# Optimization experiments

Hardware: AMD Instinct MI355X
Metric: run time of the kernel (lower is better)

## Reference

```python
import jax, jax.numpy as jnp
from jax import lax
import numpy as np

P = 128      # stored adversarial patch resolution
WIN = 256    # max pasted-patch extent (>= max patch_size = sqrt(300*300*0.4) ~ 190)
MINH = 60.0  # min_patch_height
H, W, B, N = 896, 896, 8, 24


def _bilinear(img, ys, xs):
    """Bilinearly sample img [h,w,c] on the grid ys x xs -> [len(ys), len(xs), c]."""
    h, w = img.shape[0], img.shape[1]
    ys = jnp.clip(ys, 0.0, h - 1.0)
    xs = jnp.clip(xs, 0.0, w - 1.0)
    y0 = jnp.floor(ys); x0 = jnp.floor(xs)
    y0i = y0.astype(jnp.int32); x0i = x0.astype(jnp.int32)
    y1i = jnp.minimum(y0i + 1, h - 1); x1i = jnp.minimum(x0i + 1, w - 1)
    wy = (ys - y0)[:, None, None]; wx = (xs - x0)[None, :, None]
    v00 = img[y0i][:, x0i]; v01 = img[y0i][:, x1i]
    v10 = img[y1i][:, x0i]; v11 = img[y1i][:, x1i]
    return (1 - wy) * ((1 - wx) * v00 + wx * v01) + wy * ((1 - wx) * v10 + wx * v11)


def setup_inputs() -> dict:
    key = jax.random.key(0)
    ks = jax.random.split(key, 8)
    ymin = jax.random.uniform(ks[0], (B, N), minval=0.0, maxval=H - 320.0)
    bh = jax.random.uniform(ks[1], (B, N), minval=80.0, maxval=300.0)
    xmin = jax.random.uniform(ks[2], (B, N), minval=0.0, maxval=W - 320.0)
    bw = jax.random.uniform(ks[3], (B, N), minval=80.0, maxval=300.0)
    boxes = jnp.stack([ymin, xmin, ymin + bh, xmin + bw], axis=-1)
    images = jax.random.uniform(ks[4], (B, H, W, 3))
    patch = jax.random.uniform(ks[5], (P, P, 3))
    Ws = jax.random.normal(ks[6], (2, 1)) * 0.5
    bs = jnp.zeros((1,), jnp.float32)
    Wg = jax.random.normal(ks[7], (2, P * P)) * 0.5
    bg = jnp.zeros((P * P,), jnp.float32)
    return {"boxes": boxes, "images": images, "patch": patch,
            "Ws": Ws, "bs": bs, "Wg": Wg, "bg": bg}


def reference(boxes, images, patch, Ws, bs, Wg, bg):
    Bx, Hx, Wx, C = images.shape
    Hf, Wf = float(Hx), float(Wx)
    mu_p = patch.mean((0, 1)); sd_p = patch.std((0, 1)) + 1e-6

    def per_image(image, bxs):
        bh = (bxs[:, 2] - bxs[:, 0]) / Hf
        bw = (bxs[:, 3] - bxs[:, 1]) / Wf
        feats = jnp.stack([bh, bw], axis=-1)                      # [N,2]
        scales = jax.nn.sigmoid(feats @ Ws + bs)[:, 0] * 0.4
        # Patcher.create (vectorized over boxes)
        h = bxs[:, 2] - bxs[:, 0]; w = bxs[:, 3] - bxs[:, 1]
        ps = jnp.floor(jnp.sqrt(h * w * scales))                  # square patch side
        oy = bxs[:, 0] + h / 2.0; ox = bxs[:, 1] + w / 2.0
        ymp = jnp.maximum(oy - ps / 2.0, 0.0)
        xmp = jnp.maximum(ox - ps / 2.0, 0.0)
        ymp = jnp.where(ymp + ps > Hf, Hf - ps, ymp)
        xmp = jnp.where(xmp + ps > Wf, Wf - ps, xmp)
        pboxes = jnp.stack([ymp, xmp, ps, ps], axis=-1)           # [N,4]
        valid = ps > MINH                                          # filter-by-mask
        masks = jax.nn.sigmoid(feats @ Wg + bg).reshape(-1, P, P, 1)  # gen masks
        img_p = jnp.pad(image, ((0, WIN), (0, WIN), (0, 0)))

        def body(carry, inp):
            imgc, bgl = carry
            pbox, mask, vld = inp
            yi = pbox[0].astype(jnp.int32); xi = pbox[1].astype(jnp.int32)
            ph = pbox[2].astype(jnp.int32); pw = pbox[3].astype(jnp.int32)
            phf = jnp.maximum(ph, 1).astype(jnp.float32)
            pwf = jnp.maximum(pw, 1).astype(jnp.float32)
            # crop background region -> fixed PxP
            ys = yi.astype(jnp.float32) + (jnp.arange(P, dtype=jnp.float32) + 0.5) * phf / P - 0.5
            xs = xi.astype(jnp.float32) + (jnp.arange(P, dtype=jnp.float32) + 0.5) * pwf / P - 0.5
            patch_bg = _bilinear(imgc, ys, xs)                    # [P,P,C]
            # histogram (moment) matching of patch to local background
            mu_b = patch_bg.mean((0, 1)); sd_b = patch_bg.std((0, 1)) + 1e-6
            matched = (patch - mu_p) / sd_p * sd_b + mu_b
            blended = jnp.where(mask > 0.5, matched, patch_bg)
            r = jnp.arange(WIN, dtype=jnp.float32)
            sy = (r + 0.5) * P / phf - 0.5
            sx = (r + 0.5) * P / pwf - 0.5
            im_win = _bilinear(blended, sy, sx)
            win = lax.dynamic_slice(imgc, (yi, xi, 0), (WIN, WIN, imgc.shape[-1]))
            inside = (jnp.arange(WIN)[:, None] < ph) & (jnp.arange(WIN)[None, :] < pw) & vld
            upd = jnp.where(inside[..., None], im_win, win)
            imgc = lax.dynamic_update_slice(imgc, upd, (yi, xi, 0))
            bgl = bgl + jnp.where(vld, mask.mean(), 0.0)          # generator.bg_loss
            return (imgc, bgl), None

        (img_p, bgl), _ = lax.scan(body, (img_p, jnp.zeros((), jnp.float32)),
                                   (pboxes, masks, valid))
        # scale loss over valid boxes: mean + 0.5*variance
        vf = valid.astype(jnp.float32)
        n = jnp.maximum(vf.sum(), 1.0)
        m = (scales * vf).sum() / n
        var = (vf * (scales - m) ** 2).sum() / n
        return img_p[:Hx, :Wx], bgl + m + 0.5 * var

    out, losses = jax.vmap(per_image)(images, boxes)
    return out, losses.sum()
```

## Files before the change

### kernel.cpp

```cpp
#include <hip/hip_runtime.h>

#define PPX  128
#define PP2  16384
#define IMH  896
#define IMW  896
#define NB   24
#define NI   8
#define HP   1152
#define WP   1152
#define MAXG 6
#define NMB  (NI*NB*8)
#define NCPY 2048
#define M1   12

#define WS_BOX  8
#define WS_MASK 2048
#define WS_SCH  100352
#define WS_LIST 100608
#define WS_MSUM 101760
#define WS_PART 103424
#define WS_PBG  140288

__device__ __forceinline__ void box_geom(const float* __restrict__ bx,
    const float* __restrict__ Wsc, const float* __restrict__ bsc,
    float& scale, float& ps, int& yi, int& xi, int& ph, int& vld)
{
  float ya=bx[0], xa=bx[1], yb=bx[2], xb=bx[3];
  float bh=(yb-ya)/(float)IMH, bw=(xb-xa)/(float)IMW;
  float z = bh*Wsc[0]+bw*Wsc[1]+bsc[0];
  float sig = 1.f/(1.f+expf(-z));
  scale = sig*0.4f;
  float h=yb-ya, w=xb-xa;
  ps = floorf(sqrtf((h*w)*scale));
  float oy=ya+h*0.5f, ox=xa+w*0.5f;
  float ymp=fmaxf(oy-ps*0.5f,0.f), xmp=fmaxf(ox-ps*0.5f,0.f);
  if (ymp+ps>(float)IMH) ymp=(float)IMH-ps;
  if (xmp+ps>(float)IMW) xmp=(float)IMW-ps;
  yi=(int)ymp; xi=(int)xmp; ph=(int)ps;
  vld = (ps>60.f) ? 1 : 0;
}

__device__ __forceinline__ void analytic3(int rr, int cc, float phf,
    const float* __restrict__ pbg1, const float* __restrict__ patch,
    const unsigned* msk, const float* ab, float v[3])
{
  float sy = ((rr + 0.5f)*128.0f)/phf - 0.5f;
  float sx = ((cc + 0.5f)*128.0f)/phf - 0.5f;
  sy = fminf(fmaxf(sy, 0.f), 127.f);
  sx = fminf(fmaxf(sx, 0.f), 127.f);
  float fy0 = floorf(sy), fx0 = floorf(sx);
  int py0 = (int)fy0, px0 = (int)fx0;
  int py1 = py0 + 1 < 127 ? py0 + 1 : 127;
  int px1 = px0 + 1 < 127 ? px0 + 1 : 127;
  float wy = sy - fy0, wx = sx - fx0;
  int i00 = (py0<<7)+px0, i01 = (py0<<7)+px1, i10 = (py1<<7)+px0, i11 = (py1<<7)+px1;
  bool m00 = (msk[i00>>5] >> (i00&31)) & 1u;
  bool m01 = (msk[i01>>5] >> (i01&31)) & 1u;
  bool m10 = (msk[i10>>5] >> (i10&31)) & 1u;
  bool m11 = (msk[i11>>5] >> (i11&31)) & 1u;
  #pragma unroll
  for (int ch = 0; ch < 3; ++ch) {
    float a = ab[ch], be = ab[3+ch];
    float t00 = m00 ? patch[i00*3+ch]*a + be : pbg1[i00*3+ch];
    float t01 = m01 ? patch[i01*3+ch]*a + be : pbg1[i01*3+ch];
    float t10 = m10 ? patch[i10*3+ch]*a + be : pbg1[i10*3+ch];
    float t11 = m11 ? patch[i11*3+ch]*a + be : pbg1[i11*3+ch];
    v[ch] = (1.f-wy)*((1.f-wx)*t00 + wx*t01) + wy*((1.f-wx)*t10 + wx*t11);
  }
}

__device__ __forceinline__ void crop_plain(
    const float* __restrict__ src, float* __restrict__ ws, int b, int n, int blk,
    float (*s_red)[6])
{
  const int tid = threadIdx.x;
  const int* bi = (const int*)(ws + WS_BOX + (b*NB + n)*8);
  const int yi = bi[2], xi = bi[3], ph = bi[4];
  const float phf = (float)(ph > 1 ? ph : 1);
  float* __restrict__ pbg = ws + WS_PBG + (size_t)(b*NB + n)*PP2*3;
  float sm[3] = {0,0,0}, sq[3] = {0,0,0};
  #pragma unroll
  for (int k = 0; k < 2; ++k) {
    int idx = blk*512 + k*256 + tid;
    int py = idx >> 7, px = idx & 127;
    float ys = ((float)yi + (py + 0.5f)*phf*(1.0f/PPX)) - 0.5f;
    float xs = ((float)xi + (px + 0.5f)*phf*(1.0f/PPX)) - 0.5f;
    ys = fminf(fmaxf(ys, 0.f), (float)(HP-1));
    xs = fminf(fmaxf(xs, 0.f), (float)(WP-1));
    float fy0 = floorf(ys), fx0 = floorf(xs);
    int y0 = (int)fy0, x0 = (int)fx0;
    int y1 = y0 + 1 < HP-1 ? y0 + 1 : HP-1;
    int x1 = x0 + 1 < WP-1 ? x0 + 1 : WP-1;
    float wy = ys - fy0, wx = xs - fx0;
    bool y0i = y0 < IMH, y1i = y1 < IMH, x0i = x0 < IMW, x1i = x1 < IMW;
    const float* r0 = src + (size_t)y0*IMW*3;
    const float* r1 = src + (size_t)y1*IMW*3;
    #pragma unroll
    for (int c = 0; c < 3; ++c) {
      float v00 = (y0i && x0i) ? r0[x0*3+c] : 0.f;
      float v01 = (y0i && x1i) ? r0[x1*3+c] : 0.f;
      float v10 = (y1i && x0i) ? r1[x0*3+c] : 0.f;
      float v11 = (y1i && x1i) ? r1[x1*3+c] : 0.f;
      float v = (1.f-wy)*((1.f-wx)*v00 + wx*v01) + wy*((1.f-wx)*v10 + wx*v11);
      pbg[idx*3+c] = v;
      sm[c] += v; sq[c] += v*v;
    }
  }
  float vals[6] = {sm[0],sm[1],sm[2],sq[0],sq[1],sq[2]};
  #pragma unroll
  for (int off = 32; off; off >>= 1)
    #pragma unroll
    for (int k = 0; k < 6; ++k) vals[k] += __shfl_down(vals[k], off);
  int wid = tid >> 6;
  __syncthreads();
  if ((tid & 63) == 0)
    for (int k = 0; k < 6; ++k) s_red[wid][k] = vals[k];
  __syncthreads();
  if (tid == 0) {
    float* part = ws + WS_PART + (size_t)((b*NB + n)*32 + blk)*6;
    for (int k = 0; k < 6; ++k)
      part[k] = s_red[0][k] + s_red[1][k] + s_red[2][k] + s_red[3][k];
  }
}

__global__ __launch_bounds__(256) void sched_k(
    const float* __restrict__ boxes,
    const float* __restrict__ Wsc, const float* __restrict__ bsc,
    const float* __restrict__ patch, float* __restrict__ ws)
{
  const int tid = threadIdx.x;
  if (blockIdx.x == 1) {
    __shared__ float s_red6[256][6];
    float s0=0,s1=0,s2=0,q0=0,q1=0,q2=0;
    for (int i = tid; i < PP2; i += 256) {
      float a = patch[i*3+0], b = patch[i*3+1], c = patch[i*3+2];
      s0+=a; s1+=b; s2+=c; q0+=a*a; q1+=b*b; q2+=c*c;
    }
    s_red6[tid][0]=s0; s_red6[tid][1]=s1; s_red6[tid][2]=s2;
    s_red6[tid][3]=q0; s_red6[tid][4]=q1; s_red6[tid][5]=q2;
    __syncthreads();
    for (int s = 128; s > 0; s >>= 1) {
      if (tid < s)
        for (int k=0;k<6;++k) s_red6[tid][k] += s_red6[tid+s][k];
      __syncthreads();
    }
    if (tid == 0) {
      for (int c=0;c<3;++c) {
        float mu  = s_red6[0][c]   * (1.0f/PP2);
        float var = s_red6[0][3+c] * (1.0f/PP2) - mu*mu;
        float sd  = sqrtf(fmaxf(var, 0.f)) + 1e-6f;
        ws[c] = mu; ws[3+c] = sd;
      }
    }
    return;
  }
  __shared__ int g_yi[NI*NB], g_xi[NI*NB], g_ph[NI*NB], g_vl[NI*NB];
  if (tid < NI*NB) {
    float scale, ps; int yi, xi, ph, vld;
    box_geom(boxes + tid*4, Wsc, bsc, scale, ps, yi, xi, ph, vld);
    g_yi[tid]=yi; g_xi[tid]=xi; g_ph[tid]=ph; g_vl[tid]=vld;
    float* bst = ws + WS_BOX + tid*8;
    bst[0] = scale;
    bst[1] = ps;
    ((int*)bst)[2] = yi;
    ((int*)bst)[3] = xi;
    ((int*)bst)[4] = ph;
    bst[5] = vld ? 1.f : 0.f;
  }
  __syncthreads();
  if (tid < NI) {
    unsigned* sch = ((unsigned*)ws) + WS_SCH + tid*32;
    unsigned* lst = ((unsigned*)ws) + WS_LIST + tid*(MAXG*NB);
    int lv[NB];
    int cnt[MAXG];
    for (int L = 0; L < MAXG; ++L) cnt[L] = 0;
    for (int n = 0; n < NB; ++n) {
      int idx = tid*NB + n;
      if (!g_vl[idx]) { lv[n] = -1; sch[n] = 255u; continue; }
      int y0 = g_yi[idx]-2, y1 = g_yi[idx]+g_ph[idx]+3;
      int x0 = g_xi[idx]-2, x1 = g_xi[idx]+g_ph[idx]+3;
      int L = 0;
      for (int m = 0; m < n; ++m) {
        if (lv[m] < 0) continue;
        int mi = tid*NB + m;
        int my0 = g_yi[mi]-2, my1 = g_yi[mi]+g_ph[mi]+3;
        int mx0 = g_xi[mi]-2, mx1 = g_xi[mi]+g_ph[mi]+3;
        if (y0 < my1 && my0 < y1 && x0 < mx1 && mx0 < x1)
          L = max(L, lv[m] + 1);
      }
      lv[n] = L;
      sch[n] = (unsigned)L;
      if (L < MAXG) lst[L*NB + cnt[L]++] = (unsigned)n;
    }
    for (int L = 0; L < MAXG; ++L) sch[24 + L] = (unsigned)cnt[L];
  }
}

__global__ __launch_bounds__(256) void first_k(
    float* __restrict__ out, const float* __restrict__ images,
    const float* __restrict__ boxes,
    const float* __restrict__ Wg, const float* __restrict__ bgv,
    float* __restrict__ ws)
{
  const int bid = blockIdx.x, tid = threadIdx.x;
  if (bid < NCPY) {
    const float4* src4 = (const float4*)images;
    float4* dst4 = (float4*)out;
    const int n4 = NI*IMH*IMW*3/4;
    for (int i = bid*256 + tid; i < n4; i += NCPY*256) dst4[i] = src4[i];
    return;
  }
  if (bid < NCPY + NMB) {
    const int w = bid - NCPY;
    const int bn = w >> 3, q = w & 7;
    float bh = (boxes[bn*4+2]-boxes[bn*4+0])/(float)IMH;
    float bw = (boxes[bn*4+3]-boxes[bn*4+1])/(float)IMW;
    unsigned* mwords = ((unsigned*)ws) + WS_MASK + bn*512;
    float lsum = 0.f;
    const int lane = tid & 63;
    #pragma unroll
    for (int i = 0; i < 8; ++i) {
      int p = q*2048 + i*256 + tid;
      float zz = bh*Wg[p] + bw*Wg[PP2 + p] + bgv[p];
      lsum += 1.0f / (1.0f + expf(-zz));
      unsigned long long m = __ballot(zz > 0.0f);
      if (lane == 0) {
        int base = p >> 5;
        mwords[base]   = (unsigned)(m & 0xffffffffULL);
        mwords[base+1] = (unsigned)(m >> 32);
      }
    }
    #pragma unroll
    for (int off = 32; off; off >>= 1) lsum += __shfl_down(lsum, off);
    __shared__ float s_r[4];
    if ((tid & 63) == 0) s_r[tid >> 6] = lsum;
    __syncthreads();
    if (tid == 0) ws[WS_MSUM + bn*8 + q] = s_r[0] + s_r[1] + s_r[2] + s_r[3];
    return;
  }
  const int w = bid - NCPY - NMB;
  const int b = w / (M1*32);
  const int rem = w - b*(M1*32);
  const int j = rem >> 5, blk = rem & 31;
  __shared__ float s_red[4][6];
  __shared__ int s_cn[NB];
  __shared__ int s_cc;
  const unsigned* sch = ((const unsigned*)ws) + WS_SCH + b*32;
  if (tid == 0) s_cc = (int)sch[24 + 0];
  __syncthreads();
  const int cc = s_cc;
  if (j >= cc) return;
  if (tid < cc) s_cn[tid] = (int)(((const unsigned*)ws) + WS_LIST + b*(MAXG*NB))[tid];
  __syncthreads();
  const float* src = images + (size_t)b*IMH*IMW*3;
  for (int jj = j; jj < cc; jj += M1)
    crop_plain(src, ws, b, s_cn[jj], blk, s_red);
}

__global__ __launch_bounds__(256) void crop_k(
    float* __restrict__ out, float* __restrict__ ws, int L, int M)
{
  const int bid = blockIdx.x, tid = threadIdx.x;
  const int b = bid / (M*32);
  const int rem = bid - b*(M*32);
  const int j = rem >> 5, blk = rem & 31;
  __shared__ float s_red[4][6];
  __shared__ int s_cn[NB];
  __shared__ int s_cc;
  const unsigned* sch = ((const unsigned*)ws) + WS_SCH + b*32;
  if (tid == 0) s_cc = (int)sch[24 + L];
  __syncthreads();
  const int cc = s_cc;
  if (j >= cc) return;
  if (tid < cc) s_cn[tid] = (int)(((const unsigned*)ws) + WS_LIST + b*(MAXG*NB))[L*NB + tid];
  __syncthreads();
  const float* src = out + (size_t)b*IMH*IMW*3;
  for (int jj = j; jj < cc; jj += M)
    crop_plain(src, ws, b, s_cn[jj], blk, s_red);
}

__global__ __launch_bounds__(256) void paste_k(
    float* __restrict__ out, const float* __restrict__ patch,
    float* __restrict__ ws, int L, int M)
{
  const int bid = blockIdx.x, tid = threadIdx.x;
  if (bid >= NI*M*32) {
    if (tid == 0) {
      float total = 0.f;
      for (int b = 0; b < NI; ++b) {
        float sum_s = 0.f, cnt = 0.f, bgl = 0.f;
        for (int n = 0; n < NB; ++n) {
          const float* bst = ws + WS_BOX + (b*NB + n)*8;
          float v = bst[5];
          float msum = 0.f;
          for (int q = 0; q < 8; ++q) msum += ws[WS_MSUM + (b*NB + n)*8 + q];
          sum_s += bst[0]*v; cnt += v; bgl += (msum*(1.0f/PP2))*v;
        }
        float nn = fmaxf(cnt, 1.0f);
        float m = sum_s / nn;
        float var = 0.f;
        for (int n = 0; n < NB; ++n) {
          const float* bst = ws + WS_BOX + (b*NB + n)*8;
          float d = bst[0] - m;
          var += bst[5]*d*d;
        }
        var /= nn;
        total += bgl + m + 0.5f*var;
      }
      out[(size_t)NI*IMH*IMW*3] = total;
    }
    return;
  }
  const int b = bid / (M*32);
  const int rem = bid - b*(M*32);
  const int j = rem >> 5, r = rem & 31;
  __shared__ int s_cp;
  __shared__ int s_pn[NB];
  __shared__ float s_ab[6];
  __shared__ unsigned s_mask[512];
  const unsigned* sch = ((const unsigned*)ws) + WS_SCH + b*32;
  if (tid == 0) s_cp = (int)sch[24 + L];
  __syncthreads();
  const int cp = s_cp;
  if (j >= cp) return;
  if (tid < cp) s_pn[tid] = (int)(((const unsigned*)ws) + WS_LIST + b*(MAXG*NB))[L*NB + tid];
  __syncthreads();
  float* __restrict__ img = out + (size_t)b*IMH*IMW*3;

  for (int jj = j; jj < cp; jj += M) {
    const int n = s_pn[jj];
    if (tid < 32) {
      const float* part = ws + WS_PART + (size_t)((b*NB + n)*32 + tid)*6;
      float v[6];
      #pragma unroll
      for (int k = 0; k < 6; ++k) v[k] = part[k];
      #pragma unroll
      for (int off = 16; off; off >>= 1)
        #pragma unroll
        for (int k = 0; k < 6; ++k) v[k] += __shfl_down(v[k], off, 32);
      if (tid == 0) {
        #pragma unroll
        for (int c = 0; c < 3; ++c) {
          float mu  = v[c]   * (1.0f/PP2);
          float var = v[3+c] * (1.0f/PP2) - mu*mu;
          float sd  = sqrtf(fmaxf(var, 0.f)) + 1e-6f;
          float alpha = sd / ws[3+c];
          s_ab[c]   = alpha;
          s_ab[3+c] = mu - ws[c]*alpha;
        }
      }
    }
    {
      const unsigned* mwords = ((const unsigned*)ws) + WS_MASK + (b*NB + n)*512;
      s_mask[tid]       = mwords[tid];
      s_mask[tid + 256] = mwords[tid + 256];
    }
    __syncthreads();
    const int* bi = (const int*)(ws + WS_BOX + (b*NB + n)*8);
    const int yi = bi[2], xi = bi[3], ph = bi[4];
    const float phf = (float)(ph > 1 ? ph : 1);
    const float* pbgp = ws + WS_PBG + (size_t)(b*NB + n)*PP2*3;
    const int tot = ph*ph;
    const int chunk = (tot + 31) / 32;
    const int i0 = r*chunk;
    const int i1 = min(tot, i0 + chunk);
    for (int idx = i0 + tid; idx < i1; idx += 256) {
      int rr = (int)((unsigned)idx / (unsigned)ph);
      int cx = idx - rr*ph;
      float v[3];
      analytic3(rr, cx, phf, pbgp, patch, s_mask, s_ab, v);
      float* dst = img + ((size_t)(yi + rr)*IMW + (xi + cx))*3;
      dst[0] = v[0]; dst[1] = v[1]; dst[2] = v[2];
    }
    __syncthreads();
  }
}

__global__ __launch_bounds__(256) void fallback_k(
    float* __restrict__ out, const float* __restrict__ patch, float* __restrict__ ws)
{
  const int b = blockIdx.x, tid = threadIdx.x;
  const unsigned* sch = ((const unsigned*)ws) + WS_SCH + b*32;
  float* __restrict__ img = out + (size_t)b*IMH*IMW*3;
  float* __restrict__ pbg = ws + WS_PBG + (size_t)(b*NB + 0)*PP2*3;
  __shared__ float s_red6[256][6];
  __shared__ float s_ab[6];
  __shared__ unsigned s_mask[512];

  for (int n = 0; n < NB; ++n) {
    unsigned g = sch[n];
    if (g < (unsigned)MAXG || g == 255u) continue;
    const float* bst = ws + WS_BOX + (b*NB + n)*8;
    const int yi = ((const int*)bst)[2];
    const int xi = ((const int*)bst)[3];
    const int ph = ((const int*)bst)[4];
    const float phf = (float)(ph > 1 ? ph : 1);

    float sm[3]={0,0,0}, sq[3]={0,0,0};
    for (int k = 0; k < PP2/256; ++k) {
      int idx = k*256 + tid;
      int py = idx >> 7, px = idx & 127;
      float ys = ((float)yi + (py + 0.5f)*phf*(1.0f/PPX)) - 0.5f;
      float xs = ((float)xi + (px + 0.5f)*phf*(1.0f/PPX)) - 0.5f;
      ys = fminf(fmaxf(ys, 0.f), (float)(HP-1));
      xs = fminf(fmaxf(xs, 0.f), (float)(WP-1));
      float fy0 = floorf(ys), fx0 = floorf(xs);
      int y0 = (int)fy0, x0 = (int)fx0;
      int y1 = y0 + 1 < HP-1 ? y0 + 1 : HP-1;
      int x1 = x0 + 1 < WP-1 ? x0 + 1 : WP-1;
      float wy = ys - fy0, wx = xs - fx0;
      bool y0i = y0 < IMH, y1i = y1 < IMH, x0i = x0 < IMW, x1i = x1 < IMW;
      const float* r0 = img + (size_t)y0*IMW*3;
      const float* r1 = img + (size_t)y1*IMW*3;
      #pragma unroll
      for (int c = 0; c < 3; ++c) {
        float v00 = (y0i && x0i) ? r0[x0*3+c] : 0.f;
        float v01 = (y0i && x1i) ? r0[x1*3+c] : 0.f;
        float v10 = (y1i && x0i) ? r1[x0*3+c] : 0.f;
        float v11 = (y1i && x1i) ? r1[x1*3+c] : 0.f;
        float v = (1.f-wy)*((1.f-wx)*v00 + wx*v01) + wy*((1.f-wx)*v10 + wx*v11);
        pbg[idx*3+c] = v;
        sm[c] += v; sq[c] += v*v;
      }
    }
    s_red6[tid][0]=sm[0]; s_red6[tid][1]=sm[1]; s_red6[tid][2]=sm[2];
    s_red6[tid][3]=sq[0]; s_red6[tid][4]=sq[1]; s_red6[tid][5]=sq[2];
    __syncthreads();
    for (int s2 = 128; s2 > 0; s2 >>= 1) {
      if (tid < s2)
        for (int k=0;k<6;++k) s_red6[tid][k] += s_red6[tid+s2][k];
      __syncthreads();
    }
    if (tid == 0) {
      for (int c=0;c<3;++c) {
        float mu  = s_red6[0][c]   * (1.0f/PP2);
        float var = s_red6[0][3+c] * (1.0f/PP2) - mu*mu;
        float sd  = sqrtf(fmaxf(var, 0.f)) + 1e-6f;
        float alpha = sd / ws[3+c];
        s_ab[c]   = alpha;
        s_ab[3+c] = mu - ws[c]*alpha;
      }
    }
    {
      const unsigned* mwords = ((const unsigned*)ws) + WS_MASK + (b*NB + n)*512;
      s_mask[tid]       = mwords[tid];
      s_mask[tid + 256] = mwords[tid + 256];
    }
    __syncthreads();
    const int tot = ph*ph;
    for (int idx = tid; idx < tot; idx += 256) {
      int rr = (int)((unsigned)idx / (unsigned)ph);
      int cc = idx - rr*ph;
      float v[3];
      analytic3(rr, cc, phf, pbg, patch, s_mask, s_ab, v);
      float* dst = img + ((size_t)(yi + rr)*IMW + (xi + cc))*3;
      dst[0] = v[0]; dst[1] = v[1]; dst[2] = v[2];
    }
    __syncthreads();
  }
}

extern "C" void kernel_launch(void* const* d_in, const int* in_sizes, int n_in,
                              void* d_out, int out_size, void* d_ws, size_t ws_size,
                              hipStream_t stream) {
  const float* boxes  = (const float*)d_in[0];
  const float* images = (const float*)d_in[1];
  const float* patch  = (const float*)d_in[2];
  const float* Wsc    = (const float*)d_in[3];
  const float* bsc    = (const float*)d_in[4];
  const float* Wg     = (const float*)d_in[5];
  const float* bgv    = (const float*)d_in[6];
  float* out = (float*)d_out;
  float* ws  = (float*)d_ws;

  sched_k<<<2, 256, 0, stream>>>(boxes, Wsc, bsc, patch, ws);
  first_k<<<NCPY + NMB + NI*M1*32, 256, 0, stream>>>(out, images, boxes, Wg, bgv, ws);
  paste_k<<<NI*M1*32 + 1, 256, 0, stream>>>(out, patch, ws, 0, M1);
  crop_k <<<NI*8*32, 256, 0, stream>>>(out, ws, 1, 8);
  paste_k<<<NI*8*32, 256, 0, stream>>>(out, patch, ws, 1, 8);
  crop_k <<<NI*4*32, 256, 0, stream>>>(out, ws, 2, 4);
  paste_k<<<NI*4*32, 256, 0, stream>>>(out, patch, ws, 2, 4);
  crop_k <<<NI*2*32, 256, 0, stream>>>(out, ws, 3, 2);
  paste_k<<<NI*2*32, 256, 0, stream>>>(out, patch, ws, 3, 2);
  crop_k <<<NI*2*32, 256, 0, stream>>>(out, ws, 4, 2);
  paste_k<<<NI*2*32, 256, 0, stream>>>(out, patch, ws, 4, 2);
  crop_k <<<NI*2*32, 256, 0, stream>>>(out, ws, 5, 2);
  paste_k<<<NI*2*32, 256, 0, stream>>>(out, patch, ws, 5, 2);
  fallback_k<<<NI, 256, 0, stream>>>(out, patch, ws);
}
```

Measured before the change: 200.8 us.

## Fuse crop and paste per level into single 1024-thread step kernel

Merges the scheduling kernel into the copy/mask kernel, and fuses each level's crop (background resample plus statistics) and paste into one step kernel. That kernel uses one 1024-thread block per box instead of 32 crop blocks and 32 paste blocks. This removes the partial-sum workspace round trip and cuts the launch count roughly in half. In exchange, each box now gets a single block, so far fewer blocks are in flight per level, and the per-level block counts were also retuned.

```diff
diff --git a/kernel.cpp b/kernel.cpp
--- a/kernel.cpp
+++ b/kernel.cpp
@@ -9,17 +9,15 @@
 #define HP   1152
 #define WP   1152
 #define MAXG 6
-#define NMB  (NI*NB*8)
+#define NMB  (NI*NB)
 #define NCPY 2048
-#define M1   12
 
 #define WS_BOX  8
 #define WS_MASK 2048
 #define WS_SCH  100352
 #define WS_LIST 100608
 #define WS_MSUM 101760
-#define WS_PART 103424
-#define WS_PBG  140288
+#define WS_PBG  103424
 
 __device__ __forceinline__ void box_geom(const float* __restrict__ bx,
     const float* __restrict__ Wsc, const float* __restrict__ bsc,
@@ -69,67 +67,15 @@
   }
 }
 
-__device__ __forceinline__ void crop_plain(
-    const float* __restrict__ src, float* __restrict__ ws, int b, int n, int blk,
-    float (*s_red)[6])
-{
-  const int tid = threadIdx.x;
-  const int* bi = (const int*)(ws + WS_BOX + (b*NB + n)*8);
-  const int yi = bi[2], xi = bi[3], ph = bi[4];
-  const float phf = (float)(ph > 1 ? ph : 1);
-  float* __restrict__ pbg = ws + WS_PBG + (size_t)(b*NB + n)*PP2*3;
-  float sm[3] = {0,0,0}, sq[3] = {0,0,0};
-  #pragma unroll
-  for (int k = 0; k < 2; ++k) {
-    int idx = blk*512 + k*256 + tid;
-    int py = idx >> 7, px = idx & 127;
-    float ys = ((float)yi + (py + 0.5f)*phf*(1.0f/PPX)) - 0.5f;
-    float xs = ((float)xi + (px + 0.5f)*phf*(1.0f/PPX)) - 0.5f;
-    ys = fminf(fmaxf(ys, 0.f), (float)(HP-1));
-    xs = fminf(fmaxf(xs, 0.f), (float)(WP-1));
-    float fy0 = floorf(ys), fx0 = floorf(xs);
-    int y0 = (int)fy0, x0 = (int)fx0;
-    int y1 = y0 + 1 < HP-1 ? y0 + 1 : HP-1;
-    int x1 = x0 + 1 < WP-1 ? x0 + 1 : WP-1;
-    float wy = ys - fy0, wx = xs - fx0;
-    bool y0i = y0 < IMH, y1i = y1 < IMH, x0i = x0 < IMW, x1i = x1 < IMW;
-    const float* r0 = src + (size_t)y0*IMW*3;
-    const float* r1 = src + (size_t)y1*IMW*3;
-    #pragma unroll
-    for (int c = 0; c < 3; ++c) {
-      float v00 = (y0i && x0i) ? r0[x0*3+c] : 0.f;
-      float v01 = (y0i && x1i) ? r0[x1*3+c] : 0.f;
-      float v10 = (y1i && x0i) ? r1[x0*3+c] : 0.f;
-      float v11 = (y1i && x1i) ? r1[x1*3+c] : 0.f;
-      float v = (1.f-wy)*((1.f-wx)*v00 + wx*v01) + wy*((1.f-wx)*v10 + wx*v11);
-      pbg[idx*3+c] = v;
-      sm[c] += v; sq[c] += v*v;
-    }
-  }
-  float vals[6] = {sm[0],sm[1],sm[2],sq[0],sq[1],sq[2]};
-  #pragma unroll
-  for (int off = 32; off; off >>= 1)
-    #pragma unroll
-    for (int k = 0; k < 6; ++k) vals[k] += __shfl_down(vals[k], off);
-  int wid = tid >> 6;
-  __syncthreads();
-  if ((tid & 63) == 0)
-    for (int k = 0; k < 6; ++k) s_red[wid][k] = vals[k];
-  __syncthreads();
-  if (tid == 0) {
-    float* part = ws + WS_PART + (size_t)((b*NB + n)*32 + blk)*6;
-    for (int k = 0; k < 6; ++k)
-      part[k] = s_red[0][k] + s_red[1][k] + s_red[2][k] + s_red[3][k];
-  }
-}
-
-__global__ __launch_bounds__(256) void sched_k(
+__global__ __launch_bounds__(256) void first_k(
+    float* __restrict__ out, const float* __restrict__ images,
     const float* __restrict__ boxes,
     const float* __restrict__ Wsc, const float* __restrict__ bsc,
+    const float* __restrict__ Wg, const float* __restrict__ bgv,
     const float* __restrict__ patch, float* __restrict__ ws)
 {
-  const int tid = threadIdx.x;
-  if (blockIdx.x == 1) {
+  const int bid = blockIdx.x, tid = threadIdx.x;
+  if (bid == NCPY) {
     __shared__ float s_red6[256][6];
     float s0=0,s1=0,s2=0,q0=0,q1=0,q2=0;
     for (int i = tid; i < PP2; i += 256) {
@@ -154,65 +100,52 @@
     }
     return;
   }
-  __shared__ int g_yi[NI*NB], g_xi[NI*NB], g_ph[NI*NB], g_vl[NI*NB];
-  if (tid < NI*NB) {
-    float scale, ps; int yi, xi, ph, vld;
-    box_geom(boxes + tid*4, Wsc, bsc, scale, ps, yi, xi, ph, vld);
-    g_yi[tid]=yi; g_xi[tid]=xi; g_ph[tid]=ph; g_vl[tid]=vld;
-    float* bst = ws + WS_BOX + tid*8;
-    bst[0] = scale;
-    bst[1] = ps;
-    ((int*)bst)[2] = yi;
-    ((int*)bst)[3] = xi;
-    ((int*)bst)[4] = ph;
-    bst[5] = vld ? 1.f : 0.f;
-  }
-  __syncthreads();
-  if (tid < NI) {
-    unsigned* sch = ((unsigned*)ws) + WS_SCH + tid*32;
-    unsigned* lst = ((unsigned*)ws) + WS_LIST + tid*(MAXG*NB);
-    int lv[NB];
-    int cnt[MAXG];
-    for (int L = 0; L < MAXG; ++L) cnt[L] = 0;
-    for (int n = 0; n < NB; ++n) {
-      int idx = tid*NB + n;
-      if (!g_vl[idx]) { lv[n] = -1; sch[n] = 255u; continue; }
-      int y0 = g_yi[idx]-2, y1 = g_yi[idx]+g_ph[idx]+3;
-      int x0 = g_xi[idx]-2, x1 = g_xi[idx]+g_ph[idx]+3;
-      int L = 0;
-      for (int m = 0; m < n; ++m) {
-        if (lv[m] < 0) continue;
-        int mi = tid*NB + m;
-        int my0 = g_yi[mi]-2, my1 = g_yi[mi]+g_ph[mi]+3;
-        int mx0 = g_xi[mi]-2, mx1 = g_xi[mi]+g_ph[mi]+3;
-        if (y0 < my1 && my0 < y1 && x0 < mx1 && mx0 < x1)
-          L = max(L, lv[m] + 1);
-      }
-      lv[n] = L;
-      sch[n] = (unsigned)L;
-      if (L < MAXG) lst[L*NB + cnt[L]++] = (unsigned)n;
-    }
-    for (int L = 0; L < MAXG; ++L) sch[24 + L] = (unsigned)cnt[L];
-  }
-}
-
-__global__ __launch_bounds__(256) void first_k(
-    float* __restrict__ out, const float* __restrict__ images,
-    const float* __restrict__ boxes,
-    const float* __restrict__ Wg, const float* __restrict__ bgv,
-    float* __restrict__ ws)
-{
-  const int bid = blockIdx.x, tid = threadIdx.x;
-  if (bid < NCPY) {
-    const float4* src4 = (const float4*)images;
-    float4* dst4 = (float4*)out;
-    const int n4 = NI*IMH*IMW*3/4;
-    for (int i = bid*256 + tid; i < n4; i += NCPY*256) dst4[i] = src4[i];
+  if (bid == NCPY + 1) {
+    __shared__ int g_yi[NI*NB], g_xi[NI*NB], g_ph[NI*NB], g_vl[NI*NB];
+    if (tid < NI*NB) {
+      float scale, ps; int yi, xi, ph, vld;
+      box_geom(boxes + tid*4, Wsc, bsc, scale, ps, yi, xi, ph, vld);
+      g_yi[tid]=yi; g_xi[tid]=xi; g_ph[tid]=ph; g_vl[tid]=vld;
+      float* bst = ws + WS_BOX + tid*8;
+      bst[0] = scale;
+      bst[1] = ps;
+      ((int*)bst)[2] = yi;
+      ((int*)bst)[3] = xi;
+      ((int*)bst)[4] = ph;
+      bst[5] = vld ? 1.f : 0.f;
+    }
+    __syncthreads();
+    if (tid < NI) {
+      unsigned* sch = ((unsigned*)ws) + WS_SCH + tid*32;
+      unsigned* lst = ((unsigned*)ws) + WS_LIST + tid*(MAXG*NB);
+      int lv[NB];
+      int cnt[MAXG];
+      for (int L = 0; L < MAXG; ++L) cnt[L] = 0;
+      for (int n = 0; n < NB; ++n) {
+        int idx = tid*NB + n;
+        if (!g_vl[idx]) { lv[n] = -1; sch[n] = 255u; continue; }
+        int y0 = g_yi[idx]-2, y1 = g_yi[idx]+g_ph[idx]+3;
+        int x0 = g_xi[idx]-2, x1 = g_xi[idx]+g_ph[idx]+3;
+        int L = 0;
+        for (int m = 0; m < n; ++m) {
+          if (lv[m] < 0) continue;
+          int mi = tid*NB + m;
+          int my0 = g_yi[mi]-2, my1 = g_yi[mi]+g_ph[mi]+3;
+          int mx0 = g_xi[mi]-2, mx1 = g_xi[mi]+g_ph[mi]+3;
+          if (y0 < my1 && my0 < y1 && x0 < mx1 && mx0 < x1)
+            L = max(L, lv[m] + 1);
+        }
+        lv[n] = L;
+        sch[n] = (unsigned)L;
+        if (L < MAXG) lst[L*NB + cnt[L]++] = (unsigned)n;
+      }
+      for (int L = 0; L < MAXG; ++L) sch[24 + L] = (unsigned)cnt[L];
+    }
     return;
   }
-  if (bid < NCPY + NMB) {
-    const int w = bid - NCPY;
-    const int bn = w >> 3, q = w & 7;
+
+  if (bid < NMB*8) {
+    const int bn = bid >> 3, q = bid & 7;
     float bh = (boxes[bn*4+2]-boxes[bn*4+0])/(float)IMH;
     float bw = (boxes[bn*4+3]-boxes[bn*4+1])/(float)IMW;
     unsigned* mwords = ((unsigned*)ws) + WS_MASK + bn*512;
@@ -236,73 +169,47 @@
     if ((tid & 63) == 0) s_r[tid >> 6] = lsum;
     __syncthreads();
     if (tid == 0) ws[WS_MSUM + bn*8 + q] = s_r[0] + s_r[1] + s_r[2] + s_r[3];
-    return;
-  }
-  const int w = bid - NCPY - NMB;
-  const int b = w / (M1*32);
-  const int rem = w - b*(M1*32);
-  const int j = rem >> 5, blk = rem & 31;
-  __shared__ float s_red[4][6];
-  __shared__ int s_cn[NB];
-  __shared__ int s_cc;
-  const unsigned* sch = ((const unsigned*)ws) + WS_SCH + b*32;
-  if (tid == 0) s_cc = (int)sch[24 + 0];
-  __syncthreads();
-  const int cc = s_cc;
-  if (j >= cc) return;
-  if (tid < cc) s_cn[tid] = (int)(((const unsigned*)ws) + WS_LIST + b*(MAXG*NB))[tid];
-  __syncthreads();
-  const float* src = images + (size_t)b*IMH*IMW*3;
-  for (int jj = j; jj < cc; jj += M1)
-    crop_plain(src, ws, b, s_cn[jj], blk, s_red);
-}
-
-__global__ __launch_bounds__(256) void crop_k(
-    float* __restrict__ out, float* __restrict__ ws, int L, int M)
-{
-  const int bid = blockIdx.x, tid = threadIdx.x;
-  const int b = bid / (M*32);
-  const int rem = bid - b*(M*32);
-  const int j = rem >> 5, blk = rem & 31;
-  __shared__ float s_red[4][6];
-  __shared__ int s_cn[NB];
-  __shared__ int s_cc;
-  const unsigned* sch = ((const unsigned*)ws) + WS_SCH + b*32;
-  if (tid == 0) s_cc = (int)sch[24 + L];
-  __syncthreads();
-  const int cc = s_cc;
-  if (j >= cc) return;
-  if (tid < cc) s_cn[tid] = (int)(((const unsigned*)ws) + WS_LIST + b*(MAXG*NB))[L*NB + tid];
-  __syncthreads();
-  const float* src = out + (size_t)b*IMH*IMW*3;
-  for (int jj = j; jj < cc; jj += M)
-    crop_plain(src, ws, b, s_cn[jj], blk, s_red);
-}
-
-__global__ __launch_bounds__(256) void paste_k(
+  }
+
+  {
+    const float4* src4 = (const float4*)images;
+    float4* dst4 = (float4*)out;
+    const int n4 = NI*IMH*IMW*3/4;
+    for (int i = bid*256 + tid; i < n4; i += NCPY*256) dst4[i] = src4[i];
+  }
+}
+
+__global__ __launch_bounds__(1024) void step_k(
     float* __restrict__ out, const float* __restrict__ patch,
     float* __restrict__ ws, int L, int M)
 {
   const int bid = blockIdx.x, tid = threadIdx.x;
-  if (bid >= NI*M*32) {
+  if (bid >= NI*M) {
+    __shared__ float l_sc[NI*NB], l_ms[NI*NB], l_vl[NI*NB];
+    if (tid < NI*NB) {
+      const float* bst = ws + WS_BOX + tid*8;
+      l_sc[tid] = bst[0]; l_vl[tid] = bst[5];
+      float ms = 0.f;
+      for (int q = 0; q < 8; ++q) ms += ws[WS_MSUM + tid*8 + q];
+      l_ms[tid] = ms;
+    }
+    __syncthreads();
     if (tid == 0) {
       float total = 0.f;
       for (int b = 0; b < NI; ++b) {
         float sum_s = 0.f, cnt = 0.f, bgl = 0.f;
         for (int n = 0; n < NB; ++n) {
-          const float* bst = ws + WS_BOX + (b*NB + n)*8;
-          float v = bst[5];
-          float msum = 0.f;
-          for (int q = 0; q < 8; ++q) msum += ws[WS_MSUM + (b*NB + n)*8 + q];
-          sum_s += bst[0]*v; cnt += v; bgl += (msum*(1.0f/PP2))*v;
+          int idx = b*NB + n;
+          float v = l_vl[idx];
+          sum_s += l_sc[idx]*v; cnt += v; bgl += (l_ms[idx]*(1.0f/PP2))*v;
         }
         float nn = fmaxf(cnt, 1.0f);
         float m = sum_s / nn;
         float var = 0.f;
         for (int n = 0; n < NB; ++n) {
-          const float* bst = ws + WS_BOX + (b*NB + n)*8;
-          float d = bst[0] - m;
-          var += bst[5]*d*d;
+          int idx = b*NB + n;
+          float d = l_sc[idx] - m;
+          var += l_vl[idx]*d*d;
         }
         var /= nn;
         total += bgl + m + 0.5f*var;
@@ -311,94 +218,35 @@
     }
     return;
   }
-  const int b = bid / (M*32);
-  const int rem = bid - b*(M*32);
-  const int j = rem >> 5, r = rem & 31;
-  __shared__ int s_cp;
-  __shared__ int s_pn[NB];
+
+  const int b = bid / M, j = bid - (bid / M)*M;
+  __shared__ int s_cnt;
+  __shared__ int s_mem[NB];
+  __shared__ float s_red[16][6];
   __shared__ float s_ab[6];
   __shared__ unsigned s_mask[512];
+
   const unsigned* sch = ((const unsigned*)ws) + WS_SCH + b*32;
-  if (tid == 0) s_cp = (int)sch[24 + L];
+  if (tid == 0) s_cnt = (int)sch[24 + L];
   __syncthreads();
-  const int cp = s_cp;
-  if (j >= cp) return;
-  if (tid < cp) s_pn[tid] = (int)(((const unsigned*)ws) + WS_LIST + b*(MAXG*NB))[L*NB + tid];
+  const int cnt = s_cnt;
+  if (j >= cnt) return;
+  if (tid < cnt) s_mem[tid] = (int)(((const unsigned*)ws) + WS_LIST + b*(MAXG*NB))[L*NB + tid];
   __syncthreads();
+
   float* __restrict__ img = out + (size_t)b*IMH*IMW*3;
 
-  for (int jj = j; jj < cp; jj += M) {
-    const int n = s_pn[jj];
-    if (tid < 32) {
-      const float* part = ws + WS_PART + (size_t)((b*NB + n)*32 + tid)*6;
-      float v[6];
-      #pragma unroll
-      for (int k = 0; k < 6; ++k) v[k] = part[k];
-      #pragma unroll
-      for (int off = 16; off; off >>= 1)
-        #pragma unroll
-        for (int k = 0; k < 6; ++k) v[k] += __shfl_down(v[k], off, 32);
-      if (tid == 0) {
-        #pragma unroll
-        for (int c = 0; c < 3; ++c) {
-          float mu  = v[c]   * (1.0f/PP2);
-          float var = v[3+c] * (1.0f/PP2) - mu*mu;
-          float sd  = sqrtf(fmaxf(var, 0.f)) + 1e-6f;
-          float alpha = sd / ws[3+c];
-          s_ab[c]   = alpha;
-          s_ab[3+c] = mu - ws[c]*alpha;
-        }
-      }
-    }
-    {
-      const unsigned* mwords = ((const unsigned*)ws) + WS_MASK + (b*NB + n)*512;
-      s_mask[tid]       = mwords[tid];
-      s_mask[tid + 256] = mwords[tid + 256];
-    }
-    __syncthreads();
+  for (int jj = j; jj < cnt; jj += M) {
+    const int n = s_mem[jj];
     const int* bi = (const int*)(ws + WS_BOX + (b*NB + n)*8);
     const int yi = bi[2], xi = bi[3], ph = bi[4];
     const float phf = (float)(ph > 1 ? ph : 1);
-    const float* pbgp = ws + WS_PBG + (size_t)(b*NB + n)*PP2*3;
-    const int tot = ph*ph;
-    const int chunk = (tot + 31) / 32;
-    const int i0 = r*chunk;
-    const int i1 = min(tot, i0 + chunk);
-    for (int idx = i0 + tid; idx < i1; idx += 256) {
-      int rr = (int)((unsigned)idx / (unsigned)ph);
-      int cx = idx - rr*ph;
-      float v[3];
-      analytic3(rr, cx, phf, pbgp, patch, s_mask, s_ab, v);
-      float* dst = img + ((size_t)(yi + rr)*IMW + (xi + cx))*3;
-      dst[0] = v[0]; dst[1] = v[1]; dst[2] = v[2];
-    }
-    __syncthreads();
-  }
-}
-
-__global__ __launch_bounds__(256) void fallback_k(
-    float* __restrict__ out, const float* __restrict__ patch, float* __restrict__ ws)
-{
-  const int b = blockIdx.x, tid = threadIdx.x;
-  const unsigned* sch = ((const unsigned*)ws) + WS_SCH + b*32;
-  float* __restrict__ img = out + (size_t)b*IMH*IMW*3;
-  float* __restrict__ pbg = ws + WS_PBG + (size_t)(b*NB + 0)*PP2*3;
-  __shared__ float s_red6[256][6];
-  __shared__ float s_ab[6];
-  __shared__ unsigned s_mask[512];
-
-  for (int n = 0; n < NB; ++n) {
-    unsigned g = sch[n];
-    if (g < (unsigned)MAXG || g == 255u) continue;
-    const float* bst = ws + WS_BOX + (b*NB + n)*8;
-    const int yi = ((const int*)bst)[2];
-    const int xi = ((const int*)bst)[3];
-    const int ph = ((const int*)bst)[4];
-    const float phf = (float)(ph > 1 ? ph : 1);
-
-    float sm[3]={0,0,0}, sq[3]={0,0,0};
-    for (int k = 0; k < PP2/256; ++k) {
-      int idx = k*256 + tid;
+    float* __restrict__ pbg = ws + WS_PBG + (size_t)(b*NB + n)*PP2*3;
+
+    float sm[3] = {0,0,0}, sq[3] = {0,0,0};
+    #pragma unroll
+    for (int k = 0; k < PP2/1024; ++k) {
+      int idx = k*1024 + tid;
       int py = idx >> 7, px = idx & 127;
       float ys = ((float)yi + (py + 0.5f)*phf*(1.0f/PPX)) - 0.5f;
       float xs = ((float)xi + (px + 0.5f)*phf*(1.0f/PPX)) - 0.5f;
@@ -423,32 +271,120 @@
         sm[c] += v; sq[c] += v*v;
       }
     }
-    s_red6[tid][0]=sm[0]; s_red6[tid][1]=sm[1]; s_red6[tid][2]=sm[2];
-    s_red6[tid][3]=sq[0]; s_red6[tid][4]=sq[1]; s_red6[tid][5]=sq[2];
-    __syncthreads();
-    for (int s2 = 128; s2 > 0; s2 >>= 1) {
-      if (tid < s2)
-        for (int k=0;k<6;++k) s_red6[tid][k] += s_red6[tid+s2][k];
-      __syncthreads();
-    }
+    float vals[6] = {sm[0],sm[1],sm[2],sq[0],sq[1],sq[2]};
+    #pragma unroll
+    for (int off = 32; off; off >>= 1)
+      #pragma unroll
+      for (int k = 0; k < 6; ++k) vals[k] += __shfl_down(vals[k], off);
+    if ((tid & 63) == 0)
+      for (int k = 0; k < 6; ++k) s_red[tid >> 6][k] = vals[k];
+    if (tid < 512) {
+      const unsigned* mwords = ((const unsigned*)ws) + WS_MASK + (b*NB + n)*512;
+      s_mask[tid] = mwords[tid];
+    }
+    __syncthreads();
     if (tid == 0) {
-      for (int c=0;c<3;++c) {
-        float mu  = s_red6[0][c]   * (1.0f/PP2);
-        float var = s_red6[0][3+c] * (1.0f/PP2) - mu*mu;
+      float acc[6] = {0,0,0,0,0,0};
+      for (int w2 = 0; w2 < 16; ++w2)
+        for (int k = 0; k < 6; ++k) acc[k] += s_red[w2][k];
+      for (int c = 0; c < 3; ++c) {
+        float mu  = acc[c]   * (1.0f/PP2);
+        float var = acc[3+c] * (1.0f/PP2) - mu*mu;
         float sd  = sqrtf(fmaxf(var, 0.f)) + 1e-6f;
         float alpha = sd / ws[3+c];
         s_ab[c]   = alpha;
         s_ab[3+c] = mu - ws[c]*alpha;
       }
     }
-    {
+    __syncthreads();
+
+    const int tot = ph*ph;
+    for (int idx = tid; idx < tot; idx += 1024) {
+      int rr = (int)((unsigned)idx / (unsigned)ph);
+      int cx = idx - rr*ph;
+      float v[3];
+      analytic3(rr, cx, phf, pbg, patch, s_mask, s_ab, v);
+      float* dst = img + ((size_t)(yi + rr)*IMW + (xi + cx))*3;
+      dst[0] = v[0]; dst[1] = v[1]; dst[2] = v[2];
+    }
+    __syncthreads();
+  }
+}
+
+__global__ __launch_bounds__(1024) void fb_k(
+    float* __restrict__ out, const float* __restrict__ patch, float* __restrict__ ws)
+{
+  const int b = blockIdx.x, tid = threadIdx.x;
+  const unsigned* sch = ((const unsigned*)ws) + WS_SCH + b*32;
+  __shared__ float s_red[16][6];
+  __shared__ float s_ab[6];
+  __shared__ unsigned s_mask[512];
+  float* __restrict__ img = out + (size_t)b*IMH*IMW*3;
+
+  for (int n = 0; n < NB; ++n) {
+    unsigned g = sch[n];
+    if (g < (unsigned)MAXG || g == 255u) continue;
+    const int* bi = (const int*)(ws + WS_BOX + (b*NB + n)*8);
+    const int yi = bi[2], xi = bi[3], ph = bi[4];
+    const float phf = (float)(ph > 1 ? ph : 1);
+    float* __restrict__ pbg = ws + WS_PBG + (size_t)(b*NB + n)*PP2*3;
+
+    float sm[3]={0,0,0}, sq[3]={0,0,0};
+    #pragma unroll
+    for (int k = 0; k < PP2/1024; ++k) {
+      int idx = k*1024 + tid;
+      int py = idx >> 7, px = idx & 127;
+      float ys = ((float)yi + (py + 0.5f)*phf*(1.0f/PPX)) - 0.5f;
+      float xs = ((float)xi + (px + 0.5f)*phf*(1.0f/PPX)) - 0.5f;
+      ys = fminf(fmaxf(ys, 0.f), (float)(HP-1));
+      xs = fminf(fmaxf(xs, 0.f), (float)(WP-1));
+      float fy0 = floorf(ys), fx0 = floorf(xs);
+      int y0 = (int)fy0, x0 = (int)fx0;
+      int y1 = y0 + 1 < HP-1 ? y0 + 1 : HP-1;
+      int x1 = x0 + 1 < WP-1 ? x0 + 1 : WP-1;
+      float wy = ys - fy0, wx = xs - fx0;
+      bool y0i = y0 < IMH, y1i = y1 < IMH, x0i = x0 < IMW, x1i = x1 < IMW;
+      const float* r0 = img + (size_t)y0*IMW*3;
+      const float* r1 = img + (size_t)y1*IMW*3;
+      #pragma unroll
+      for (int c = 0; c < 3; ++c) {
+        float v00 = (y0i && x0i) ? r0[x0*3+c] : 0.f;
+        float v01 = (y0i && x1i) ? r0[x1*3+c] : 0.f;
+        float v10 = (y1i && x0i) ? r1[x0*3+c] : 0.f;
+        float v11 = (y1i && x1i) ? r1[x1*3+c] : 0.f;
+        float v = (1.f-wy)*((1.f-wx)*v00 + wx*v01) + wy*((1.f-wx)*v10 + wx*v11);
+        pbg[idx*3+c] = v;
+        sm[c] += v; sq[c] += v*v;
+      }
+    }
+    float vals[6] = {sm[0],sm[1],sm[2],sq[0],sq[1],sq[2]};
+    #pragma unroll
+    for (int off = 32; off; off >>= 1)
+      #pragma unroll
+      for (int k = 0; k < 6; ++k) vals[k] += __shfl_down(vals[k], off);
+    if ((tid & 63) == 0)
+      for (int k = 0; k < 6; ++k) s_red[tid >> 6][k] = vals[k];
+    if (tid < 512) {
       const unsigned* mwords = ((const unsigned*)ws) + WS_MASK + (b*NB + n)*512;
-      s_mask[tid]       = mwords[tid];
-      s_mask[tid + 256] = mwords[tid + 256];
+      s_mask[tid] = mwords[tid];
+    }
+    __syncthreads();
+    if (tid == 0) {
+      float acc[6] = {0,0,0,0,0,0};
+      for (int w2 = 0; w2 < 16; ++w2)
+        for (int k = 0; k < 6; ++k) acc[k] += s_red[w2][k];
+      for (int c = 0; c < 3; ++c) {
+        float mu  = acc[c]   * (1.0f/PP2);
+        float var = acc[3+c] * (1.0f/PP2) - mu*mu;
+        float sd  = sqrtf(fmaxf(var, 0.f)) + 1e-6f;
+        float alpha = sd / ws[3+c];
+        s_ab[c]   = alpha;
+        s_ab[3+c] = mu - ws[c]*alpha;
+      }
     }
     __syncthreads();
     const int tot = ph*ph;
-    for (int idx = tid; idx < tot; idx += 256) {
+    for (int idx = tid; idx < tot; idx += 1024) {
       int rr = (int)((unsigned)idx / (unsigned)ph);
       int cc = idx - rr*ph;
       float v[3];
@@ -473,18 +409,12 @@
   float* out = (float*)d_out;
   float* ws  = (float*)d_ws;
 
-  sched_k<<<2, 256, 0, stream>>>(boxes, Wsc, bsc, patch, ws);
-  first_k<<<NCPY + NMB + NI*M1*32, 256, 0, stream>>>(out, images, boxes, Wg, bgv, ws);
-  paste_k<<<NI*M1*32 + 1, 256, 0, stream>>>(out, patch, ws, 0, M1);
-  crop_k <<<NI*8*32, 256, 0, stream>>>(out, ws, 1, 8);
-  paste_k<<<NI*8*32, 256, 0, stream>>>(out, patch, ws, 1, 8);
-  crop_k <<<NI*4*32, 256, 0, stream>>>(out, ws, 2, 4);
-  paste_k<<<NI*4*32, 256, 0, stream>>>(out, patch, ws, 2, 4);
-  crop_k <<<NI*2*32, 256, 0, stream>>>(out, ws, 3, 2);
-  paste_k<<<NI*2*32, 256, 0, stream>>>(out, patch, ws, 3, 2);
-  crop_k <<<NI*2*32, 256, 0, stream>>>(out, ws, 4, 2);
-  paste_k<<<NI*2*32, 256, 0, stream>>>(out, patch, ws, 4, 2);
-  crop_k <<<NI*2*32, 256, 0, stream>>>(out, ws, 5, 2);
-  paste_k<<<NI*2*32, 256, 0, stream>>>(out, patch, ws, 5, 2);
-  fallback_k<<<NI, 256, 0, stream>>>(out, patch, ws);
-}
+  first_k<<<NCPY + 2, 256, 0, stream>>>(out, images, boxes, Wsc, bsc, Wg, bgv, patch, ws);
+  step_k<<<NI*12 + 1, 1024, 0, stream>>>(out, patch, ws, 0, 12);
+  step_k<<<NI*8,      1024, 0, stream>>>(out, patch, ws, 1, 8);
+  step_k<<<NI*6,      1024, 0, stream>>>(out, patch, ws, 2, 6);
+  step_k<<<NI*6,      1024, 0, stream>>>(out, patch, ws, 3, 6);
+  step_k<<<NI*4,      1024, 0, stream>>>(out, patch, ws, 4, 4);
+  step_k<<<NI*4,      1024, 0, stream>>>(out, patch, ws, 5, 4);
+  fb_k<<<NI, 1024, 0, stream>>>(out, patch, ws);
+}
```

New measurement: 489.1 us. 2.44x slower.
